# Kernel tuning notes

Measured on AMD Instinct MI355X. Metric: run time of the kernel, lower is better.

The kernel has to match this reference:

```python
import jax, jax.numpy as jnp
import numpy as np

M, N = 32, 32
IN_MULT, OUT_MULT = 5, 40
HQ = M * M  # 1024, hidden size of GRU_Q and GRU_Sigma; GRU_S hidden = N*N = 1024


def _l2norm(x):
    # torch F.normalize(p=2, dim=0, eps=1e-12)
    return x / jnp.maximum(jnp.linalg.norm(x), 1e-12)


def _gru(x, h, Wih, Whh, bih, bhh):
    # single-step torch nn.GRU cell, gate order r,z,n
    gi = Wih @ x + bih
    gh = Whh @ h + bhh
    Hh = h.shape[0]
    r = jax.nn.sigmoid(gi[:Hh] + gh[:Hh])
    z = jax.nn.sigmoid(gi[Hh:2 * Hh] + gh[Hh:2 * Hh])
    n = jnp.tanh(gi[2 * Hh:] + r * gh[2 * Hh:])
    return (1.0 - z) * n + z * h


def setup_inputs() -> dict:
    key = jax.random.key(0)
    ks = iter(jax.random.split(key, 48))

    def rn(shape, scale=1.0):
        return jax.random.normal(next(ks), shape, dtype=jnp.float32) * jnp.float32(scale)

    def w(o, i):
        return rn((o, i), 1.0 / np.sqrt(i))

    d_in_sigma = HQ + M * IN_MULT          # 1184
    d_in_s = N * N + 2 * N * IN_MULT       # 1344
    d_fc2_in = HQ + N * N                  # 2048
    d_fc2_hid = d_fc2_in * OUT_MULT        # 81920
    inp = dict(
        y=rn((N,)),
        m1x_posterior=rn((M, 1)), m1x_posterior_previous=rn((M, 1)),
        m1x_prior_previous=rn((M, 1)), y_previous=rn((N, 1)),
        h_Q=rn((HQ,)), h_Sigma=rn((HQ,)), h_S=rn((N * N,)),
        F=w(M, M), H=w(N, M),
        FC5_w=w(M * IN_MULT, M), FC5_b=rn((M * IN_MULT,), 0.01),
        FC6_w=w(M * IN_MULT, M), FC6_b=rn((M * IN_MULT,), 0.01),
        FC7_w=w(2 * N * IN_MULT, 2 * N), FC7_b=rn((2 * N * IN_MULT,), 0.01),
        GRUQ_Wih=w(3 * HQ, M * IN_MULT), GRUQ_Whh=w(3 * HQ, HQ),
        GRUQ_bih=rn((3 * HQ,), 0.01), GRUQ_bhh=rn((3 * HQ,), 0.01),
        GRUSig_Wih=w(3 * HQ, d_in_sigma), GRUSig_Whh=w(3 * HQ, HQ),
        GRUSig_bih=rn((3 * HQ,), 0.01), GRUSig_bhh=rn((3 * HQ,), 0.01),
        GRUS_Wih=w(3 * N * N, d_in_s), GRUS_Whh=w(3 * N * N, N * N),
        GRUS_bih=rn((3 * N * N,), 0.01), GRUS_bhh=rn((3 * N * N,), 0.01),
        FC1_w=w(N * N, HQ), FC1_b=rn((N * N,), 0.01),
        FC2_w1=w(d_fc2_hid, d_fc2_in), FC2_b1=rn((d_fc2_hid,), 0.01),
        FC2_w2=w(N * M, d_fc2_hid), FC2_b2=rn((N * M,), 0.01),
        FC3_w=w(M * M, N * N + N * M), FC3_b=rn((M * M,), 0.01),
        FC4_w=w(HQ, HQ + M * M), FC4_b=rn((HQ,), 0.01),
        fix_H_flag=1,
    )
    return inp


def _forward(y, m1x_posterior, m1x_posterior_previous, m1x_prior_previous, y_previous,
             h_Q, h_Sigma, h_S, F, H,
             FC5_w, FC5_b, FC6_w, FC6_b, FC7_w, FC7_b,
             GRUQ_Wih, GRUQ_Whh, GRUQ_bih, GRUQ_bhh,
             GRUSig_Wih, GRUSig_Whh, GRUSig_bih, GRUSig_bhh,
             GRUS_Wih, GRUS_Whh, GRUS_bih, GRUS_bhh,
             FC1_w, FC1_b, FC2_w1, FC2_b1, FC2_w2, FC2_b2,
             FC3_w, FC3_b, FC4_w, FC4_b):
    # step_prior (fix_H_flag=True path: h is linear)
    m1x_prior = F @ m1x_posterior          # [m,1]
    m1y = H @ m1x_prior                    # [n,1]
    # step_KGain_est: feature differences, L2-normalized
    obs_diff = _l2norm(y - y_previous[:, 0])
    obs_innov_diff = _l2norm(y - m1y[:, 0])
    fw_evol_diff = _l2norm(m1x_posterior[:, 0] - m1x_posterior_previous[:, 0])
    fw_update_diff = _l2norm(m1x_posterior[:, 0] - m1x_prior_previous[:, 0])
    # KGain_step (dropout layers are identity in eval)
    out_FC5 = jax.nn.relu(FC5_w @ fw_evol_diff + FC5_b)
    out_Q = _gru(out_FC5, h_Q, GRUQ_Wih, GRUQ_Whh, GRUQ_bih, GRUQ_bhh)
    out_FC6 = jax.nn.relu(FC6_w @ fw_update_diff + FC6_b)
    out_Sigma = _gru(jnp.concatenate([out_Q, out_FC6]), h_Sigma,
                     GRUSig_Wih, GRUSig_Whh, GRUSig_bih, GRUSig_bhh)
    out_FC1 = jax.nn.relu(FC1_w @ out_Sigma + FC1_b)
    out_FC7 = jax.nn.relu(FC7_w @ jnp.concatenate([obs_diff, obs_innov_diff]) + FC7_b)
    out_S = _gru(jnp.concatenate([out_FC1, out_FC7]), h_S,
                 GRUS_Wih, GRUS_Whh, GRUS_bih, GRUS_bhh)
    in_FC2 = jnp.concatenate([out_Sigma, out_S])
    out_FC2 = FC2_w2 @ jax.nn.relu(FC2_w1 @ in_FC2 + FC2_b1) + FC2_b2   # [m*n]
    out_FC3 = jax.nn.relu(FC3_w @ jnp.concatenate([out_S, out_FC2]) + FC3_b)
    out_FC4 = jax.nn.relu(FC4_w @ jnp.concatenate([out_Sigma, out_FC3]) + FC4_b)  # new h_Sigma state
    del out_FC4  # state update only; not part of returned output
    # KNet_step update
    KG = out_FC2.reshape(M, N)
    dy = y[:, None] - m1y
    m1x_posterior_new = m1x_prior + KG @ dy
    return m1x_posterior_new[:, 0]


def reference(y, m1x_posterior, m1x_posterior_previous, m1x_prior_previous, y_previous,
              h_Q, h_Sigma, h_S, F, H,
              FC5_w, FC5_b, FC6_w, FC6_b, FC7_w, FC7_b,
              GRUQ_Wih, GRUQ_Whh, GRUQ_bih, GRUQ_bhh,
              GRUSig_Wih, GRUSig_Whh, GRUSig_bih, GRUSig_bhh,
              GRUS_Wih, GRUS_Whh, GRUS_bih, GRUS_bhh,
              FC1_w, FC1_b, FC2_w1, FC2_b1, FC2_w2, FC2_b2,
              FC3_w, FC3_b, FC4_w, FC4_b, fix_H_flag):
    return _forward(y, m1x_posterior, m1x_posterior_previous, m1x_prior_previous, y_previous,
                    h_Q, h_Sigma, h_S, F, H,
                    FC5_w, FC5_b, FC6_w, FC6_b, FC7_w, FC7_b,
                    GRUQ_Wih, GRUQ_Whh, GRUQ_bih, GRUQ_bhh,
                    GRUSig_Wih, GRUSig_Whh, GRUSig_bih, GRUSig_bhh,
                    GRUS_Wih, GRUS_Whh, GRUS_bih, GRUS_bhh,
                    FC1_w, FC1_b, FC2_w1, FC2_b1, FC2_w2, FC2_b2,
                    FC3_w, FC3_b, FC4_w, FC4_b)
```

## Files before the change

### kernel.cpp

```cpp
#include <hip/hip_runtime.h>
#include <math.h>

#define DEV __device__ __forceinline__

DEV float dot4(float4 w, float4 x) {
    float s = 0.f;
    s = fmaf(w.x, x.x, s); s = fmaf(w.y, x.y, s);
    s = fmaf(w.z, x.z, s); s = fmaf(w.w, x.w, s);
    return s;
}

DEV float wave_reduce(float v) {
    for (int off = 32; off > 0; off >>= 1) v += __shfl_down(v, off);
    return v;
}

#define WS_PRIOR   0
#define WS_DY      32
#define WS_FC5     64
#define WS_XSIG    224
#define WS_INFC2   1408
#define WS_XS      3456
#define WS_FC2OUT  4800
#define WS_HID     5824

__global__ void k_small(const float* __restrict__ y, const float* __restrict__ post,
                        const float* __restrict__ post_prev, const float* __restrict__ prior_prev,
                        const float* __restrict__ y_prev,
                        const float* __restrict__ F, const float* __restrict__ Hm,
                        const float* __restrict__ fc5w, const float* __restrict__ fc5b,
                        const float* __restrict__ fc6w, const float* __restrict__ fc6b,
                        const float* __restrict__ fc7w, const float* __restrict__ fc7b,
                        float* __restrict__ ws) {
    __shared__ float s_post[32], s_prior[32], s_m1y[32];
    __shared__ float s_diff[4][32];
    __shared__ float s_inv[4];
    __shared__ float s_evol[32], s_upd[32], s_obs[64];
    int tid = threadIdx.x;
    if (tid < 32) s_post[tid] = post[tid];
    __syncthreads();
    if (tid < 32) {
        float a = 0.f;
        for (int j = 0; j < 32; ++j) a = fmaf(F[tid * 32 + j], s_post[j], a);
        s_prior[tid] = a;
        ws[WS_PRIOR + tid] = a;
    }
    __syncthreads();
    if (tid < 32) {
        float a = 0.f;
        for (int j = 0; j < 32; ++j) a = fmaf(Hm[tid * 32 + j], s_prior[j], a);
        s_m1y[tid] = a;
    }
    __syncthreads();
    if (tid < 128) {
        int v = tid >> 5, j = tid & 31;
        float d;
        if (v == 0)      d = y[j] - y_prev[j];
        else if (v == 1) d = y[j] - s_m1y[j];
        else if (v == 2) d = post[j] - post_prev[j];
        else             d = post[j] - prior_prev[j];
        s_diff[v][j] = d;
    }
    __syncthreads();
    if (tid < 4) {
        float s = 0.f;
        for (int j = 0; j < 32; ++j) s += s_diff[tid][j] * s_diff[tid][j];
        s_inv[tid] = 1.0f / fmaxf(sqrtf(s), 1e-12f);
    }
    __syncthreads();
    if (tid < 128) {
        int v = tid >> 5, j = tid & 31;
        float nd = s_diff[v][j] * s_inv[v];
        if (v == 0)      s_obs[j] = nd;
        else if (v == 1) { s_obs[32 + j] = nd; ws[WS_DY + j] = s_diff[1][j]; }
        else if (v == 2) s_evol[j] = nd;
        else             s_upd[j] = nd;
    }
    __syncthreads();
    if (tid < 160) {
        float a = fc5b[tid];
        for (int j = 0; j < 32; ++j) a = fmaf(fc5w[tid * 32 + j], s_evol[j], a);
        ws[WS_FC5 + tid] = fmaxf(a, 0.f);
    } else {
        int i = tid - 160;
        float a = fc6b[i];
        for (int j = 0; j < 32; ++j) a = fmaf(fc6w[i * 32 + j], s_upd[j], a);
        ws[WS_XSIG + 1024 + i] = fmaxf(a, 0.f);
    }
    {
        float a = fc7b[tid];
        for (int j = 0; j < 64; ++j) a = fmaf(fc7w[tid * 64 + j], s_obs[j], a);
        ws[WS_XS + 1024 + tid] = fmaxf(a, 0.f);
    }
}

__global__ void k_gru(const float* __restrict__ x, const float* __restrict__ h,
                      const float* __restrict__ Wih, const float* __restrict__ Whh,
                      const float* __restrict__ bih, const float* __restrict__ bhh,
                      float* __restrict__ out, int Kx) {
    int wid = (blockIdx.x * blockDim.x + threadIdx.x) >> 6;
    int lane = threadIdx.x & 63;
    int K4 = Kx >> 2;
    const float4* x4 = (const float4*)x;
    const float4* W0 = (const float4*)Wih + (size_t)wid * K4;
    float ai0 = 0.f, ai1 = 0.f, ai2 = 0.f;
    for (int k = lane; k < K4; k += 64) {
        float4 xv = x4[k];
        ai0 += dot4(W0[k], xv);
        ai1 += dot4(W0[(size_t)1024 * K4 + k], xv);
        ai2 += dot4(W0[(size_t)2048 * K4 + k], xv);
    }
    const float4* h4 = (const float4*)h;
    const float4* V0 = (const float4*)Whh + (size_t)wid * 256;
    float ah0 = 0.f, ah1 = 0.f, ah2 = 0.f;
    for (int k = lane; k < 256; k += 64) {
        float4 hv = h4[k];
        ah0 += dot4(V0[k], hv);
        ah1 += dot4(V0[(size_t)1024 * 256 + k], hv);
        ah2 += dot4(V0[(size_t)2048 * 256 + k], hv);
    }
    for (int off = 32; off > 0; off >>= 1) {
        ai0 += __shfl_down(ai0, off); ai1 += __shfl_down(ai1, off); ai2 += __shfl_down(ai2, off);
        ah0 += __shfl_down(ah0, off); ah1 += __shfl_down(ah1, off); ah2 += __shfl_down(ah2, off);
    }
    if (lane == 0) {
        float gr = ai0 + bih[wid]        + ah0 + bhh[wid];
        float gz = ai1 + bih[wid + 1024] + ah1 + bhh[wid + 1024];
        float r = 1.f / (1.f + expf(-gr));
        float z = 1.f / (1.f + expf(-gz));
        float n = tanhf(ai2 + bih[wid + 2048] + r * (ah2 + bhh[wid + 2048]));
        out[wid] = (1.f - z) * n + z * h[wid];
    }
}

__global__ void k_matvec_relu(const float* __restrict__ W, const float* __restrict__ x,
                              const float* __restrict__ b, float* __restrict__ out, int K) {
    int wid = (blockIdx.x * blockDim.x + threadIdx.x) >> 6;
    int lane = threadIdx.x & 63;
    int K4 = K >> 2;
    const float4* w4 = (const float4*)W + (size_t)wid * K4;
    const float4* x4 = (const float4*)x;
    float a = 0.f;
    for (int k = lane; k < K4; k += 64) {
        a += dot4(w4[k], x4[k]);
    }
    a = wave_reduce(a);
    if (lane == 0) out[wid] = fmaxf(a + b[wid], 0.f);
}

__global__ void k_matvec_big(const float* __restrict__ W, const float* __restrict__ x,
                             const float* __restrict__ b, float* __restrict__ out, int K) {
    int row = blockIdx.x;
    int tid = threadIdx.x;
    int K4 = K >> 2;
    const float4* w4 = (const float4*)W + (size_t)row * K4;
    const float4* x4 = (const float4*)x;
    float a = 0.f;
    for (int k = tid; k < K4; k += 256) {
        a += dot4(w4[k], x4[k]);
    }
    a = wave_reduce(a);
    __shared__ float s[4];
    if ((tid & 63) == 0) s[tid >> 6] = a;
    __syncthreads();
    if (tid == 0) out[row] = s[0] + s[1] + s[2] + s[3] + b[row];
}

__global__ void k_final(const float* __restrict__ ws, float* __restrict__ out) {
    int i = threadIdx.x;
    const float* kg = ws + WS_FC2OUT;
    const float* dy = ws + WS_DY;
    float a = ws[WS_PRIOR + i];
    for (int j = 0; j < 32; ++j) a = fmaf(kg[i * 32 + j], dy[j], a);
    out[i] = a;
}

extern "C" void kernel_launch(void* const* d_in, const int* in_sizes, int n_in,
                              void* d_out, int out_size, void* d_ws, size_t ws_size,
                              hipStream_t stream) {
    const float* y          = (const float*)d_in[0];
    const float* post       = (const float*)d_in[1];
    const float* post_prev  = (const float*)d_in[2];
    const float* prior_prev = (const float*)d_in[3];
    const float* y_prev     = (const float*)d_in[4];
    const float* h_Q        = (const float*)d_in[5];
    const float* h_Sigma    = (const float*)d_in[6];
    const float* h_S        = (const float*)d_in[7];
    const float* F          = (const float*)d_in[8];
    const float* Hm         = (const float*)d_in[9];
    const float* FC5_w      = (const float*)d_in[10];
    const float* FC5_b      = (const float*)d_in[11];
    const float* FC6_w      = (const float*)d_in[12];
    const float* FC6_b      = (const float*)d_in[13];
    const float* FC7_w      = (const float*)d_in[14];
    const float* FC7_b      = (const float*)d_in[15];
    const float* GQ_Wih     = (const float*)d_in[16];
    const float* GQ_Whh     = (const float*)d_in[17];
    const float* GQ_bih     = (const float*)d_in[18];
    const float* GQ_bhh     = (const float*)d_in[19];
    const float* GS_Wih     = (const float*)d_in[20];
    const float* GS_Whh     = (const float*)d_in[21];
    const float* GS_bih     = (const float*)d_in[22];
    const float* GS_bhh     = (const float*)d_in[23];
    const float* GU_Wih     = (const float*)d_in[24];
    const float* GU_Whh     = (const float*)d_in[25];
    const float* GU_bih     = (const float*)d_in[26];
    const float* GU_bhh     = (const float*)d_in[27];
    const float* FC1_w      = (const float*)d_in[28];
    const float* FC1_b      = (const float*)d_in[29];
    const float* FC2_w1     = (const float*)d_in[30];
    const float* FC2_b1     = (const float*)d_in[31];
    const float* FC2_w2     = (const float*)d_in[32];
    const float* FC2_b2     = (const float*)d_in[33];

    float* ws = (float*)d_ws;

    k_small<<<1, 320, 0, stream>>>(y, post, post_prev, prior_prev, y_prev, F, Hm,
                                   FC5_w, FC5_b, FC6_w, FC6_b, FC7_w, FC7_b, ws);
    k_gru<<<256, 256, 0, stream>>>(ws + WS_FC5, h_Q, GQ_Wih, GQ_Whh, GQ_bih, GQ_bhh,
                                   ws + WS_XSIG, 160);
    k_gru<<<256, 256, 0, stream>>>(ws + WS_XSIG, h_Sigma, GS_Wih, GS_Whh, GS_bih, GS_bhh,
                                   ws + WS_INFC2, 1184);
    k_matvec_relu<<<256, 256, 0, stream>>>(FC1_w, ws + WS_INFC2, FC1_b, ws + WS_XS, 1024);
    k_gru<<<256, 256, 0, stream>>>(ws + WS_XS, h_S, GU_Wih, GU_Whh, GU_bih, GU_bhh,
                                   ws + WS_INFC2 + 1024, 1344);
    k_matvec_relu<<<20480, 256, 0, stream>>>(FC2_w1, ws + WS_INFC2, FC2_b1, ws + WS_HID, 2048);
    k_matvec_big<<<1024, 256, 0, stream>>>(FC2_w2, ws + WS_HID, FC2_b2, ws + WS_FC2OUT, 81920);
    k_final<<<1, 32, 0, stream>>>(ws, (float*)d_out);
}
```

Measured before the change: 211.0 us.

## Fuse small preprocessing into GRU kernels and specialize matvec loops

```diff
diff --git a/kernel.cpp b/kernel.cpp
--- a/kernel.cpp
+++ b/kernel.cpp
@@ -14,115 +14,24 @@
     for (int off = 32; off > 0; off >>= 1) v += __shfl_down(v, off);
     return v;
 }
-
-#define WS_PRIOR   0
-#define WS_DY      32
-#define WS_FC5     64
-#define WS_XSIG    224
-#define WS_INFC2   1408
-#define WS_XS      3456
-#define WS_FC2OUT  4800
-#define WS_HID     5824
-
-__global__ void k_small(const float* __restrict__ y, const float* __restrict__ post,
-                        const float* __restrict__ post_prev, const float* __restrict__ prior_prev,
-                        const float* __restrict__ y_prev,
-                        const float* __restrict__ F, const float* __restrict__ Hm,
-                        const float* __restrict__ fc5w, const float* __restrict__ fc5b,
-                        const float* __restrict__ fc6w, const float* __restrict__ fc6b,
-                        const float* __restrict__ fc7w, const float* __restrict__ fc7b,
-                        float* __restrict__ ws) {
-    __shared__ float s_post[32], s_prior[32], s_m1y[32];
-    __shared__ float s_diff[4][32];
-    __shared__ float s_inv[4];
-    __shared__ float s_evol[32], s_upd[32], s_obs[64];
-    int tid = threadIdx.x;
-    if (tid < 32) s_post[tid] = post[tid];
-    __syncthreads();
-    if (tid < 32) {
-        float a = 0.f;
-        for (int j = 0; j < 32; ++j) a = fmaf(F[tid * 32 + j], s_post[j], a);
-        s_prior[tid] = a;
-        ws[WS_PRIOR + tid] = a;
-    }
-    __syncthreads();
-    if (tid < 32) {
-        float a = 0.f;
-        for (int j = 0; j < 32; ++j) a = fmaf(Hm[tid * 32 + j], s_prior[j], a);
-        s_m1y[tid] = a;
-    }
-    __syncthreads();
-    if (tid < 128) {
-        int v = tid >> 5, j = tid & 31;
-        float d;
-        if (v == 0)      d = y[j] - y_prev[j];
-        else if (v == 1) d = y[j] - s_m1y[j];
-        else if (v == 2) d = post[j] - post_prev[j];
-        else             d = post[j] - prior_prev[j];
-        s_diff[v][j] = d;
-    }
-    __syncthreads();
-    if (tid < 4) {
-        float s = 0.f;
-        for (int j = 0; j < 32; ++j) s += s_diff[tid][j] * s_diff[tid][j];
-        s_inv[tid] = 1.0f / fmaxf(sqrtf(s), 1e-12f);
-    }
-    __syncthreads();
-    if (tid < 128) {
-        int v = tid >> 5, j = tid & 31;
-        float nd = s_diff[v][j] * s_inv[v];
-        if (v == 0)      s_obs[j] = nd;
-        else if (v == 1) { s_obs[32 + j] = nd; ws[WS_DY + j] = s_diff[1][j]; }
-        else if (v == 2) s_evol[j] = nd;
-        else             s_upd[j] = nd;
-    }
-    __syncthreads();
-    if (tid < 160) {
-        float a = fc5b[tid];
-        for (int j = 0; j < 32; ++j) a = fmaf(fc5w[tid * 32 + j], s_evol[j], a);
-        ws[WS_FC5 + tid] = fmaxf(a, 0.f);
-    } else {
-        int i = tid - 160;
-        float a = fc6b[i];
-        for (int j = 0; j < 32; ++j) a = fmaf(fc6w[i * 32 + j], s_upd[j], a);
-        ws[WS_XSIG + 1024 + i] = fmaxf(a, 0.f);
-    }
-    {
-        float a = fc7b[tid];
-        for (int j = 0; j < 64; ++j) a = fmaf(fc7w[tid * 64 + j], s_obs[j], a);
-        ws[WS_XS + 1024 + tid] = fmaxf(a, 0.f);
-    }
-}
-
-__global__ void k_gru(const float* __restrict__ x, const float* __restrict__ h,
-                      const float* __restrict__ Wih, const float* __restrict__ Whh,
-                      const float* __restrict__ bih, const float* __restrict__ bhh,
-                      float* __restrict__ out, int Kx) {
-    int wid = (blockIdx.x * blockDim.x + threadIdx.x) >> 6;
-    int lane = threadIdx.x & 63;
-    int K4 = Kx >> 2;
-    const float4* x4 = (const float4*)x;
-    const float4* W0 = (const float4*)Wih + (size_t)wid * K4;
-    float ai0 = 0.f, ai1 = 0.f, ai2 = 0.f;
-    for (int k = lane; k < K4; k += 64) {
-        float4 xv = x4[k];
-        ai0 += dot4(W0[k], xv);
-        ai1 += dot4(W0[(size_t)1024 * K4 + k], xv);
-        ai2 += dot4(W0[(size_t)2048 * K4 + k], xv);
-    }
-    const float4* h4 = (const float4*)h;
-    const float4* V0 = (const float4*)Whh + (size_t)wid * 256;
-    float ah0 = 0.f, ah1 = 0.f, ah2 = 0.f;
-    for (int k = lane; k < 256; k += 64) {
-        float4 hv = h4[k];
-        ah0 += dot4(V0[k], hv);
-        ah1 += dot4(V0[(size_t)1024 * 256 + k], hv);
-        ah2 += dot4(V0[(size_t)2048 * 256 + k], hv);
-    }
-    for (int off = 32; off > 0; off >>= 1) {
-        ai0 += __shfl_down(ai0, off); ai1 += __shfl_down(ai1, off); ai2 += __shfl_down(ai2, off);
-        ah0 += __shfl_down(ah0, off); ah1 += __shfl_down(ah1, off); ah2 += __shfl_down(ah2, off);
-    }
+DEV float reduce32(float v) {
+    for (int off = 16; off > 0; off >>= 1) v += __shfl_xor(v, off);
+    return v;
+}
+
+#define WS_Q      0
+#define WS_SIG    1024
+#define WS_S      2048
+#define WS_FC1    3072
+#define WS_HID    4096
+#define WS_KG     86016
+
+DEV void gru_tail(int wid, int lane,
+                  float ai0, float ai1, float ai2, float ah0, float ah1, float ah2,
+                  const float* __restrict__ bih, const float* __restrict__ bhh,
+                  const float* __restrict__ h, float* __restrict__ out) {
+    ai0 = wave_reduce(ai0); ai1 = wave_reduce(ai1); ai2 = wave_reduce(ai2);
+    ah0 = wave_reduce(ah0); ah1 = wave_reduce(ah1); ah2 = wave_reduce(ah2);
     if (lane == 0) {
         float gr = ai0 + bih[wid]        + ah0 + bhh[wid];
         float gz = ai1 + bih[wid + 1024] + ah1 + bhh[wid + 1024];
@@ -133,45 +42,249 @@
     }
 }
 
+DEV void gru_hh(int wid, int lane, const float* __restrict__ Whh, const float* __restrict__ h,
+                float& ah0, float& ah1, float& ah2) {
+    const float4* V = (const float4*)Whh;
+    const float4* v0 = V + (size_t)wid * 256;
+    const float4* v1 = V + (size_t)(1024 + wid) * 256;
+    const float4* v2 = V + (size_t)(2048 + wid) * 256;
+    const float4* h4 = (const float4*)h;
+#pragma unroll
+    for (int i = 0; i < 4; ++i) {
+        int k = lane + (i << 6);
+        float4 hv = h4[k];
+        ah0 += dot4(v0[k], hv); ah1 += dot4(v1[k], hv); ah2 += dot4(v2[k], hv);
+    }
+}
+
+__global__ void k_gru_q(const float* __restrict__ post, const float* __restrict__ post_prev,
+                        const float* __restrict__ fc5w, const float* __restrict__ fc5b,
+                        const float* __restrict__ h,
+                        const float* __restrict__ Wih, const float* __restrict__ Whh,
+                        const float* __restrict__ bih, const float* __restrict__ bhh,
+                        float* __restrict__ out) {
+    __shared__ __align__(16) float sx[160];
+    __shared__ float sd[32];
+    __shared__ float sinv;
+    int t = threadIdx.x;
+    if (t < 32) sd[t] = post[t] - post_prev[t];
+    __syncthreads();
+    if (t < 64) {
+        float d = (t < 32) ? sd[t] * sd[t] : 0.f;
+        d = wave_reduce(d);
+        if (t == 0) sinv = 1.f / fmaxf(sqrtf(d), 1e-12f);
+    }
+    __syncthreads();
+    if (t < 160) {
+        float a = 0.f;
+#pragma unroll
+        for (int j = 0; j < 32; ++j) a = fmaf(fc5w[t * 32 + j], sd[j], a);
+        sx[t] = fmaxf(fmaf(a, sinv, fc5b[t]), 0.f);
+    }
+    __syncthreads();
+
+    int wid = (blockIdx.x << 2) + (t >> 6);
+    int lane = t & 63;
+    const float4* W = (const float4*)Wih;
+    const float4* sx4 = (const float4*)sx;
+    float ai0 = 0.f, ai1 = 0.f, ai2 = 0.f, ah0 = 0.f, ah1 = 0.f, ah2 = 0.f;
+    if (lane < 40) {
+        float4 xv = sx4[lane];
+        ai0 = dot4(W[(size_t)wid * 40 + lane], xv);
+        ai1 = dot4(W[(size_t)(1024 + wid) * 40 + lane], xv);
+        ai2 = dot4(W[(size_t)(2048 + wid) * 40 + lane], xv);
+    }
+    gru_hh(wid, lane, Whh, h, ah0, ah1, ah2);
+    gru_tail(wid, lane, ai0, ai1, ai2, ah0, ah1, ah2, bih, bhh, h, out);
+}
+
+__global__ void k_gru_sigma(const float* __restrict__ xq,
+                            const float* __restrict__ post, const float* __restrict__ prior_prev,
+                            const float* __restrict__ fc6w, const float* __restrict__ fc6b,
+                            const float* __restrict__ h,
+                            const float* __restrict__ Wih, const float* __restrict__ Whh,
+                            const float* __restrict__ bih, const float* __restrict__ bhh,
+                            float* __restrict__ out) {
+    __shared__ __align__(16) float sx[160];
+    __shared__ float sd[32];
+    __shared__ float sinv;
+    int t = threadIdx.x;
+    if (t < 32) sd[t] = post[t] - prior_prev[t];
+    __syncthreads();
+    if (t < 64) {
+        float d = (t < 32) ? sd[t] * sd[t] : 0.f;
+        d = wave_reduce(d);
+        if (t == 0) sinv = 1.f / fmaxf(sqrtf(d), 1e-12f);
+    }
+    __syncthreads();
+    if (t < 160) {
+        float a = 0.f;
+#pragma unroll
+        for (int j = 0; j < 32; ++j) a = fmaf(fc6w[t * 32 + j], sd[j], a);
+        sx[t] = fmaxf(fmaf(a, sinv, fc6b[t]), 0.f);
+    }
+    __syncthreads();
+
+    int wid = (blockIdx.x << 2) + (t >> 6);
+    int lane = t & 63;
+    const float4* W = (const float4*)Wih;
+    const float4* w0 = W + (size_t)wid * 296;
+    const float4* w1 = W + (size_t)(1024 + wid) * 296;
+    const float4* w2 = W + (size_t)(2048 + wid) * 296;
+    const float4* q4 = (const float4*)xq;
+    const float4* sx4 = (const float4*)sx;
+    float ai0 = 0.f, ai1 = 0.f, ai2 = 0.f, ah0 = 0.f, ah1 = 0.f, ah2 = 0.f;
+#pragma unroll
+    for (int i = 0; i < 4; ++i) {
+        int k = lane + (i << 6);
+        float4 xv = q4[k];
+        ai0 += dot4(w0[k], xv); ai1 += dot4(w1[k], xv); ai2 += dot4(w2[k], xv);
+    }
+    if (lane < 40) {
+        int k = 256 + lane;
+        float4 xv = sx4[lane];
+        ai0 += dot4(w0[k], xv); ai1 += dot4(w1[k], xv); ai2 += dot4(w2[k], xv);
+    }
+    gru_hh(wid, lane, Whh, h, ah0, ah1, ah2);
+    gru_tail(wid, lane, ai0, ai1, ai2, ah0, ah1, ah2, bih, bhh, h, out);
+}
+
+__global__ void k_gru_s(const float* __restrict__ xfc1,
+                        const float* __restrict__ y, const float* __restrict__ y_prev,
+                        const float* __restrict__ post,
+                        const float* __restrict__ F, const float* __restrict__ Hm,
+                        const float* __restrict__ fc7w, const float* __restrict__ fc7b,
+                        const float* __restrict__ h,
+                        const float* __restrict__ Wih, const float* __restrict__ Whh,
+                        const float* __restrict__ bih, const float* __restrict__ bhh,
+                        float* __restrict__ out) {
+    __shared__ __align__(16) float sx[320];
+    __shared__ float sprior[32];
+    __shared__ float sd[2][32];
+    __shared__ float sinv[2];
+    int t = threadIdx.x;
+    if (t < 32) {
+        float p = 0.f;
+#pragma unroll
+        for (int j = 0; j < 32; ++j) p = fmaf(F[t * 32 + j], post[j], p);
+        sprior[t] = p;
+        sd[0][t] = y[t] - y_prev[t];
+    }
+    __syncthreads();
+    if (t < 32) {
+        float m = 0.f;
+#pragma unroll
+        for (int j = 0; j < 32; ++j) m = fmaf(Hm[t * 32 + j], sprior[j], m);
+        sd[1][t] = y[t] - m;
+    }
+    __syncthreads();
+    if (t < 64) {
+        int g = t >> 5, j = t & 31;
+        float d = sd[g][j];
+        float s = reduce32(d * d);
+        if (j == 0) sinv[g] = 1.f / fmaxf(sqrtf(s), 1e-12f);
+    }
+    __syncthreads();
+    for (int r = t; r < 320; r += 256) {
+        float a0 = 0.f, a1 = 0.f;
+#pragma unroll
+        for (int j = 0; j < 32; ++j) {
+            a0 = fmaf(fc7w[r * 64 + j], sd[0][j], a0);
+            a1 = fmaf(fc7w[r * 64 + 32 + j], sd[1][j], a1);
+        }
+        sx[r] = fmaxf(a0 * sinv[0] + a1 * sinv[1] + fc7b[r], 0.f);
+    }
+    __syncthreads();
+
+    int wid = (blockIdx.x << 2) + (t >> 6);
+    int lane = t & 63;
+    const float4* W = (const float4*)Wih;
+    const float4* w0 = W + (size_t)wid * 336;
+    const float4* w1 = W + (size_t)(1024 + wid) * 336;
+    const float4* w2 = W + (size_t)(2048 + wid) * 336;
+    const float4* x4 = (const float4*)xfc1;
+    const float4* sx4 = (const float4*)sx;
+    float ai0 = 0.f, ai1 = 0.f, ai2 = 0.f, ah0 = 0.f, ah1 = 0.f, ah2 = 0.f;
+#pragma unroll
+    for (int i = 0; i < 4; ++i) {
+        int k = lane + (i << 6);
+        float4 xv = x4[k];
+        ai0 += dot4(w0[k], xv); ai1 += dot4(w1[k], xv); ai2 += dot4(w2[k], xv);
+    }
+    {
+        int k = 256 + lane;
+        float4 xv = sx4[lane];
+        ai0 += dot4(w0[k], xv); ai1 += dot4(w1[k], xv); ai2 += dot4(w2[k], xv);
+    }
+    if (lane < 16) {
+        int k = 320 + lane;
+        float4 xv = sx4[64 + lane];
+        ai0 += dot4(w0[k], xv); ai1 += dot4(w1[k], xv); ai2 += dot4(w2[k], xv);
+    }
+    gru_hh(wid, lane, Whh, h, ah0, ah1, ah2);
+    gru_tail(wid, lane, ai0, ai1, ai2, ah0, ah1, ah2, bih, bhh, h, out);
+}
+
+template <int NITER>
 __global__ void k_matvec_relu(const float* __restrict__ W, const float* __restrict__ x,
-                              const float* __restrict__ b, float* __restrict__ out, int K) {
-    int wid = (blockIdx.x * blockDim.x + threadIdx.x) >> 6;
+                              const float* __restrict__ b, float* __restrict__ out) {
+    int wid = (blockIdx.x << 2) + (threadIdx.x >> 6);
     int lane = threadIdx.x & 63;
-    int K4 = K >> 2;
-    const float4* w4 = (const float4*)W + (size_t)wid * K4;
+    const float4* w4 = (const float4*)W + (size_t)wid * (NITER * 64);
     const float4* x4 = (const float4*)x;
-    float a = 0.f;
-    for (int k = lane; k < K4; k += 64) {
-        a += dot4(w4[k], x4[k]);
-    }
-    a = wave_reduce(a);
+    float a0 = 0.f, a1 = 0.f;
+#pragma unroll
+    for (int i = 0; i < NITER; ++i) {
+        int k = lane + (i << 6);
+        float v = dot4(w4[k], x4[k]);
+        if (i & 1) a1 += v; else a0 += v;
+    }
+    float a = wave_reduce(a0 + a1);
     if (lane == 0) out[wid] = fmaxf(a + b[wid], 0.f);
 }
 
 __global__ void k_matvec_big(const float* __restrict__ W, const float* __restrict__ x,
-                             const float* __restrict__ b, float* __restrict__ out, int K) {
+                             const float* __restrict__ b, float* __restrict__ out) {
     int row = blockIdx.x;
-    int tid = threadIdx.x;
-    int K4 = K >> 2;
-    const float4* w4 = (const float4*)W + (size_t)row * K4;
+    int t = threadIdx.x;
+    const float4* w4 = (const float4*)W + (size_t)row * 20480;
     const float4* x4 = (const float4*)x;
-    float a = 0.f;
-    for (int k = tid; k < K4; k += 256) {
-        a += dot4(w4[k], x4[k]);
-    }
-    a = wave_reduce(a);
-    __shared__ float s[4];
-    if ((tid & 63) == 0) s[tid >> 6] = a;
-    __syncthreads();
-    if (tid == 0) out[row] = s[0] + s[1] + s[2] + s[3] + b[row];
-}
-
-__global__ void k_final(const float* __restrict__ ws, float* __restrict__ out) {
+    float a0 = 0.f, a1 = 0.f;
+#pragma unroll 4
+    for (int k = t; k < 20480; k += 512) {
+        float v = dot4(w4[k], x4[k]);
+        if (k & 512) a1 += v; else a0 += v;
+    }
+    float a = wave_reduce(a0 + a1);
+    __shared__ float s[8];
+    if ((t & 63) == 0) s[t >> 6] = a;
+    __syncthreads();
+    if (t == 0) {
+        float r = b[row];
+#pragma unroll
+        for (int i = 0; i < 8; ++i) r += s[i];
+        out[row] = r;
+    }
+}
+
+__global__ void k_final(const float* __restrict__ F, const float* __restrict__ Hm,
+                        const float* __restrict__ post, const float* __restrict__ y,
+                        const float* __restrict__ kg, float* __restrict__ out) {
+    __shared__ float sprior[32], sdy[32];
     int i = threadIdx.x;
-    const float* kg = ws + WS_FC2OUT;
-    const float* dy = ws + WS_DY;
-    float a = ws[WS_PRIOR + i];
-    for (int j = 0; j < 32; ++j) a = fmaf(kg[i * 32 + j], dy[j], a);
+    float p = 0.f;
+#pragma unroll
+    for (int j = 0; j < 32; ++j) p = fmaf(F[i * 32 + j], post[j], p);
+    sprior[i] = p;
+    __syncthreads();
+    float m = 0.f;
+#pragma unroll
+    for (int j = 0; j < 32; ++j) m = fmaf(Hm[i * 32 + j], sprior[j], m);
+    sdy[i] = y[i] - m;
+    __syncthreads();
+    float a = sprior[i];
+#pragma unroll
+    for (int j = 0; j < 32; ++j) a = fmaf(kg[i * 32 + j], sdy[j], a);
     out[i] = a;
 }
 
@@ -215,16 +328,14 @@
 
     float* ws = (float*)d_ws;
 
-    k_small<<<1, 320, 0, stream>>>(y, post, post_prev, prior_prev, y_prev, F, Hm,
-                                   FC5_w, FC5_b, FC6_w, FC6_b, FC7_w, FC7_b, ws);
-    k_gru<<<256, 256, 0, stream>>>(ws + WS_FC5, h_Q, GQ_Wih, GQ_Whh, GQ_bih, GQ_bhh,
-                                   ws + WS_XSIG, 160);
-    k_gru<<<256, 256, 0, stream>>>(ws + WS_XSIG, h_Sigma, GS_Wih, GS_Whh, GS_bih, GS_bhh,
-                                   ws + WS_INFC2, 1184);
-    k_matvec_relu<<<256, 256, 0, stream>>>(FC1_w, ws + WS_INFC2, FC1_b, ws + WS_XS, 1024);
-    k_gru<<<256, 256, 0, stream>>>(ws + WS_XS, h_S, GU_Wih, GU_Whh, GU_bih, GU_bhh,
-                                   ws + WS_INFC2 + 1024, 1344);
-    k_matvec_relu<<<20480, 256, 0, stream>>>(FC2_w1, ws + WS_INFC2, FC2_b1, ws + WS_HID, 2048);
-    k_matvec_big<<<1024, 256, 0, stream>>>(FC2_w2, ws + WS_HID, FC2_b2, ws + WS_FC2OUT, 81920);
-    k_final<<<1, 32, 0, stream>>>(ws, (float*)d_out);
-}
+    k_gru_q<<<256, 256, 0, stream>>>(post, post_prev, FC5_w, FC5_b, h_Q,
+                                     GQ_Wih, GQ_Whh, GQ_bih, GQ_bhh, ws + WS_Q);
+    k_gru_sigma<<<256, 256, 0, stream>>>(ws + WS_Q, post, prior_prev, FC6_w, FC6_b, h_Sigma,
+                                         GS_Wih, GS_Whh, GS_bih, GS_bhh, ws + WS_SIG);
+    k_matvec_relu<4><<<256, 256, 0, stream>>>(FC1_w, ws + WS_SIG, FC1_b, ws + WS_FC1);
+    k_gru_s<<<256, 256, 0, stream>>>(ws + WS_FC1, y, y_prev, post, F, Hm, FC7_w, FC7_b, h_S,
+                                     GU_Wih, GU_Whh, GU_bih, GU_bhh, ws + WS_S);
+    k_matvec_relu<8><<<20480, 256, 0, stream>>>(FC2_w1, ws + WS_SIG, FC2_b1, ws + WS_HID);
+    k_matvec_big<<<1024, 512, 0, stream>>>(FC2_w2, ws + WS_HID, FC2_b2, ws + WS_KG);
+    k_final<<<1, 32, 0, stream>>>(F, Hm, post, y, ws + WS_KG, (float*)d_out);
+}
```

After: 205.6 us. -2.5%, faster.
